# Kernel tuning notes

Hardware: AMD Instinct MI355X
Metric: run time of the kernel (lower is better)

## Reference

```python
import jax, jax.numpy as jnp
import numpy as np

DIM = 512
NUM_HEADS = 8
HEAD_DIM = DIM // NUM_HEADS
SCALE = HEAD_DIM ** -0.5


def setup_inputs() -> dict:
    key = jax.random.key(0)
    k1, k2, k3, k4 = jax.random.split(key, 4)
    x = jax.random.normal(k1, (2, 4096, DIM), dtype=jnp.float32)
    # Linear weights stored as (in, out) for x @ W; torch Linear(dim, 3*dim, bias=False)
    w_qkv = jax.random.normal(k2, (DIM, 3 * DIM), dtype=jnp.float32) * (DIM ** -0.5)
    w_proj = jax.random.normal(k3, (DIM, DIM), dtype=jnp.float32) * (DIM ** -0.5)
    b_proj = jax.random.normal(k4, (DIM,), dtype=jnp.float32) * 0.02
    return {"x": x, "w_qkv": w_qkv, "w_proj": w_proj, "b_proj": b_proj}


def reference(x, w_qkv, w_proj, b_proj):
    B, N, C = x.shape
    qkv = (x @ w_qkv).reshape(B, N, 3, NUM_HEADS, HEAD_DIM)
    qkv = jnp.transpose(qkv, (2, 0, 3, 1, 4))  # (3, B, H, N, hd)
    q, k, v = qkv[0], qkv[1], qkv[2]
    attn = jnp.einsum("bhnd,bhmd->bhnm", q, k) * SCALE
    attn = jax.nn.softmax(attn, axis=-1)
    out = jnp.einsum("bhnm,bhmd->bhnd", attn, v)
    out = jnp.transpose(out, (0, 2, 1, 3)).reshape(B, N, C)
    return out @ w_proj + b_proj
```

## Files before the change

kernel.cpp:

```cpp
#include <hip/hip_runtime.h>
#include <hip/hip_bf16.h>
#include <stdint.h>
#include <math.h>

#define NC3 1536
#define QSCALE 0.18033688011111907f
#define KSPLIT 2

typedef __attribute__((ext_vector_type(8))) short short8;
typedef __attribute__((ext_vector_type(4))) short short4v;
typedef __attribute__((ext_vector_type(4))) float f32x4;
typedef __attribute__((ext_vector_type(16))) float f32x16;
typedef __attribute__((ext_vector_type(8))) _Float16 f16x8;
typedef __attribute__((ext_vector_type(2))) __fp16 fp16x2;

static __device__ __forceinline__ short f2bf(float f) {
    union { __hip_bfloat16 h; short s; } u;
    u.h = __float2bfloat16(f);
    return u.s;
}
static __device__ __forceinline__ float bf2f(short s) {
    return __uint_as_float(((unsigned)(unsigned short)s) << 16);
}
static __device__ __forceinline__ short f2h(float f) {
    union { __fp16 h; short s; } u;
    u.h = (__fp16)f;
    return u.s;
}
static __device__ __forceinline__ unsigned hpack(float a, float b) {
    union { fp16x2 h; unsigned u; } c;
    c.h = __builtin_amdgcn_cvt_pkrtz(a, b);
    return c.u;
}

#define GLD_LDS(g, l)                                                          \
    __builtin_amdgcn_global_load_lds(                                          \
        (const __attribute__((address_space(1))) void*)(g),                    \
        (__attribute__((address_space(3))) void*)(l), 16, 0, 0)

#define GSTRIDE 520
#define LADDR(row, slot) ((((row) >> 3) * GSTRIDE) + (((row) & 7) * 64) + (slot) * 8)

__global__ __launch_bounds__(256) void prep(const float* __restrict__ x,
                                            short* __restrict__ xbf,
                                            const float* __restrict__ wqkv,
                                            short* __restrict__ wqkvT,
                                            const float* __restrict__ wproj,
                                            short* __restrict__ wprojT) {
    int tx = threadIdx.x, ty = threadIdx.y;
    int tid = ty * 32 + tx;
    if (blockIdx.z == 0) {
        int bid = blockIdx.y * 48 + blockIdx.x;
        for (int i = bid * 256 + tid; i < 1048576; i += 768 * 256) {
            float4 v = ((const float4*)x)[i];
            short4v o = {f2bf(v.x), f2bf(v.y), f2bf(v.z), f2bf(v.w)};
            ((short4v*)xbf)[i] = o;
        }
        return;
    }
    const float* src;
    short* dst;
    int C;
    bool tof16;
    if (blockIdx.z == 1) { src = wqkv; dst = wqkvT; C = 1536; tof16 = false; }
    else                 { if (blockIdx.x >= 16) return; src = wproj; dst = wprojT; C = 512; tof16 = true; }
    __shared__ short t[32][33];
    int c0 = blockIdx.x * 32, r0 = blockIdx.y * 32;
#pragma unroll
    for (int i = 0; i < 4; i++) {
        float v = src[(size_t)(r0 + ty + i * 8) * C + c0 + tx];
        t[ty + i * 8][tx] = tof16 ? f2h(v) : f2bf(v);
    }
    __syncthreads();
#pragma unroll
    for (int i = 0; i < 4; i++)
        dst[(size_t)(c0 + ty + i * 8) * 512 + r0 + tx] = t[tx][ty + i * 8];
}

__global__ __launch_bounds__(256) void transpose_v(const short* __restrict__ QKV,
                                                   short* __restrict__ VT) {
    __shared__ short t[32][33];
    int n0 = blockIdx.x * 32, d0 = blockIdx.y * 32;
    int bh = blockIdx.z;
    int b = bh >> 3, h = bh & 7;
    const short* src = QKV + (size_t)b * 4096 * NC3 + 1024 + h * 64;
    short* dst = VT + (size_t)bh * 64 * 4096;
    int tx = threadIdx.x, ty = threadIdx.y;
#pragma unroll
    for (int i = 0; i < 4; i++)
        t[ty + i * 8][tx] = src[(size_t)(n0 + ty + i * 8) * NC3 + d0 + tx];
    __syncthreads();
    int ptx = (tx & ~12) | ((tx & 4) << 1) | ((tx & 8) >> 1);
#pragma unroll
    for (int i = 0; i < 4; i++)
        dst[(size_t)(d0 + ty + i * 8) * 4096 + n0 + ptx] = f2h(bf2f(t[tx][ty + i * 8]));
}

__global__ __launch_bounds__(256) void gemm_qkv(const short* __restrict__ A,
                                                const short* __restrict__ Bt,
                                                short* __restrict__ Out) {
    __shared__ __attribute__((aligned(16))) short a_sm[128 * 64];
    __shared__ __attribute__((aligned(16))) short b_sm[128 * 64];
    const int tid = threadIdx.x;
    const int lane = tid & 63;
    const int wave = tid >> 6;
    const int wr = wave >> 1, wc = wave & 1;
    const int quad = lane >> 4;
    const int l15 = lane & 15;
    const int m0 = blockIdx.x * 128;
    const int n0 = blockIdx.y * 128;
    const int srow = lane >> 3;
    const int schunk = (lane & 7) ^ srow;

    f32x4 zero4 = {0.f, 0.f, 0.f, 0.f};
    f32x4 acc[4][4];
#pragma unroll
    for (int i = 0; i < 4; i++)
#pragma unroll
        for (int j = 0; j < 4; j++) acc[i][j] = zero4;

    for (int k0 = 0; k0 < 512; k0 += 64) {
        __syncthreads();
#pragma unroll
        for (int i = 0; i < 4; i++) {
            int r0 = wave * 32 + i * 8;
            GLD_LDS(A + (size_t)(m0 + r0 + srow) * 512 + k0 + schunk * 8, a_sm + r0 * 64);
            GLD_LDS(Bt + (size_t)(n0 + r0 + srow) * 512 + k0 + schunk * 8, b_sm + r0 * 64);
        }
        __syncthreads();
#pragma unroll
        for (int kk = 0; kk < 2; kk++) {
            short8 af[4], bfr[4];
#pragma unroll
            for (int mi = 0; mi < 4; mi++) {
                int row = wr * 64 + mi * 16 + l15;
                af[mi] = *(const short8*)(a_sm + row * 64 + (((kk * 4 + quad) ^ (row & 7))) * 8);
            }
#pragma unroll
            for (int ni = 0; ni < 4; ni++) {
                int row = wc * 64 + ni * 16 + l15;
                bfr[ni] = *(const short8*)(b_sm + row * 64 + (((kk * 4 + quad) ^ (row & 7))) * 8);
            }
#pragma unroll
            for (int mi = 0; mi < 4; mi++)
#pragma unroll
                for (int ni = 0; ni < 4; ni++)
                    acc[mi][ni] = __builtin_amdgcn_mfma_f32_16x16x32_bf16(
                        af[mi], bfr[ni], acc[mi][ni], 0, 0, 0);
        }
    }

#pragma unroll
    for (int mi = 0; mi < 4; mi++) {
#pragma unroll
        for (int ni = 0; ni < 4; ni++) {
            int gm0 = m0 + wr * 64 + mi * 16 + quad * 4;
            int gn = n0 + wc * 64 + ni * 16 + l15;
            f32x4 v = acc[mi][ni];
#pragma unroll
            for (int r = 0; r < 4; r++) {
                float val = v[r];
                float o = (gn < 512) ? val * QSCALE : val;
                Out[(size_t)(gm0 + r) * NC3 + gn] = f2bf(o);
            }
        }
    }
}

__global__ __launch_bounds__(256, 4) void attn_kernel(const short* __restrict__ QKV,
                                                      const short* __restrict__ VT,
                                                      short* __restrict__ Op0,
                                                      short* __restrict__ Op1,
                                                      float* __restrict__ lpart) {
    __shared__ __attribute__((aligned(16))) short k_sm[2][8 * GSTRIDE];
    __shared__ __attribute__((aligned(16))) short v_sm[2][8 * GSTRIDE];

    const int tid = threadIdx.x;
    const int lane = tid & 63;
    const int wave = tid >> 6;
    const int l31 = lane & 31;
    const int hi = lane >> 5;
    const int qt = blockIdx.x;
    const int bh = blockIdx.y;
    const int ks = blockIdx.z;
    const int b = bh >> 3, h = bh & 7;
    const size_t tokbase = (size_t)b * 4096;
    const int rowbase = qt * 128;
    const int kt0 = ks * (64 / KSPLIT);
    const int kt1 = kt0 + (64 / KSPLIT);
    const short* Qg = QKV + h * 64;
    const short* Kg = QKV + 512 + h * 64;
    const short* VTg = VT + (size_t)bh * 64 * 4096;
    const int srow = lane >> 3;
    const int schunk = (lane & 7) ^ srow;

    short* qstage = &k_sm[0][0];
#pragma unroll
    for (int i = 0; i < 4; i++) {
        int r0 = wave * 32 + i * 8;
        GLD_LDS(Qg + (tokbase + rowbase + r0 + srow) * NC3 + schunk * 8,
                qstage + (r0 >> 3) * GSTRIDE);
    }
    __syncthreads();
    const int qrow = wave * 32 + l31;
    short8 qf[4];
#pragma unroll
    for (int kk = 0; kk < 4; kk++) {
        int slot = (kk * 2 + hi) ^ (qrow & 7);
        qf[kk] = *(const short8*)(qstage + LADDR(qrow, slot));
    }
    __syncthreads();

#pragma unroll
    for (int i = 0; i < 2; i++) {
        int r0 = wave * 16 + i * 8;
        GLD_LDS(Kg + (tokbase + (size_t)kt0 * 64 + r0 + srow) * NC3 + schunk * 8,
                k_sm[0] + (r0 >> 3) * GSTRIDE);
        GLD_LDS(VTg + (size_t)(r0 + srow) * 4096 + kt0 * 64 + schunk * 8,
                v_sm[0] + (r0 >> 3) * GSTRIDE);
    }

    const _Float16 onef = (_Float16)1.0f;
    const f16x8 ones16 = {onef, onef, onef, onef, onef, onef, onef, onef};

    f32x16 acc_o[2], acc_l;
#pragma unroll
    for (int i = 0; i < 16; i++) { acc_o[0][i] = 0.f; acc_o[1][i] = 0.f; acc_l[i] = 0.f; }

    for (int kt = kt0; kt < kt1; kt++) {
        __syncthreads();
        const int cur = kt & 1;
        if (kt < kt1 - 1) {
            const int nb = cur ^ 1;
#pragma unroll
            for (int i = 0; i < 2; i++) {
                int r0 = wave * 16 + i * 8;
                GLD_LDS(Kg + (tokbase + (size_t)(kt + 1) * 64 + r0 + srow) * NC3 + schunk * 8,
                        k_sm[nb] + (r0 >> 3) * GSTRIDE);
                GLD_LDS(VTg + (size_t)(r0 + srow) * 4096 + (kt + 1) * 64 + schunk * 8,
                        v_sm[nb] + (r0 >> 3) * GSTRIDE);
            }
        }

        f32x16 s[2];
#pragma unroll
        for (int i = 0; i < 16; i++) { s[0][i] = 0.f; s[1][i] = 0.f; }
#pragma unroll
        for (int kk = 0; kk < 4; kk++) {
#pragma unroll
            for (int kb = 0; kb < 2; kb++) {
                int row = kb * 32 + l31;
                int slot = (kk * 2 + hi) ^ (row & 7);
                short8 kf = *(const short8*)(k_sm[cur] + LADDR(row, slot));
                s[kb] = __builtin_amdgcn_mfma_f32_32x32x16_bf16(kf, qf[kk], s[kb], 0, 0, 0);
            }
        }

        unsigned pk[2][8];
#pragma unroll
        for (int kb = 0; kb < 2; kb++)
#pragma unroll
            for (int i = 0; i < 16; i += 2)
                pk[kb][i >> 1] = hpack(__builtin_amdgcn_exp2f(s[kb][i]),
                                       __builtin_amdgcn_exp2f(s[kb][i + 1]));

#pragma unroll
        for (int g = 0; g < 4; g++) {
            union { unsigned u[4]; f16x8 v; } pf;
#pragma unroll
            for (int t = 0; t < 4; t++) pf.u[t] = pk[g >> 1][4 * (g & 1) + t];
            acc_l = __builtin_amdgcn_mfma_f32_32x32x16_f16(ones16, pf.v, acc_l, 0, 0, 0);
#pragma unroll
            for (int db = 0; db < 2; db++) {
                int row = db * 32 + l31;
                int slot = (g * 2 + hi) ^ (row & 7);
                f16x8 vf = *(const f16x8*)(v_sm[cur] + LADDR(row, slot));
                acc_o[db] = __builtin_amdgcn_mfma_f32_32x32x16_f16(vf, pf.v, acc_o[db], 0, 0, 0);
            }
        }
    }

    __syncthreads();

    size_t growq = tokbase + rowbase + qrow;
    if (hi == 0) lpart[(size_t)ks * 65536 + growq * 8 + h] = acc_l[0];

    short* osm = &k_sm[0][0] + wave * 2048;
#pragma unroll
    for (int db = 0; db < 2; db++) {
#pragma unroll
        for (int i = 0; i < 16; i += 2) {
            int d = db * 32 + (i & 3) + 8 * (i >> 2) + 4 * hi;
            unsigned pkd = hpack(acc_o[db][i], acc_o[db][i + 1]);
            int slot = (d >> 3) ^ (l31 & 7);
            *(unsigned*)(osm + l31 * 64 + slot * 8 + (d & 7)) = pkd;
        }
    }
    short* Od = (ks == 0) ? Op0 : Op1;
#pragma unroll
    for (int j = 0; j < 4; j++) {
        int r = lane >> 1;
        int c = (lane & 1) * 4 + j;
        int slot = c ^ (r & 7);
        short8 ov = *(const short8*)(osm + r * 64 + slot * 8);
        size_t grow = tokbase + rowbase + wave * 32 + r;
        *(short8*)(Od + grow * 512 + h * 64 + c * 8) = ov;
    }
}

__global__ __launch_bounds__(256) void gemm_proj(const short* __restrict__ Op0,
                                                 const short* __restrict__ Op1,
                                                 const float* __restrict__ lpart,
                                                 const short* __restrict__ Bt,
                                                 float* __restrict__ OutF,
                                                 const float* __restrict__ bias) {
    __shared__ __attribute__((aligned(16))) short a0_sm[128 * 64];
    __shared__ __attribute__((aligned(16))) short a1_sm[128 * 64];
    __shared__ __attribute__((aligned(16))) short b_sm[64 * 64];
    __shared__ float linv_sm[128 * 8];
    const int tid = threadIdx.x;
    const int lane = tid & 63;
    const int wave = tid >> 6;
    const int wr = wave >> 1, wc = wave & 1;
    const int quad = lane >> 4;
    const int l15 = lane & 15;
    const int m0 = blockIdx.x * 128;
    const int n0 = blockIdx.y * 64;
    const int srow = lane >> 3;
    const int schunk = (lane & 7) ^ srow;

    {
        int idx = tid * 4;
        int row = idx >> 3;
        int hh = idx & 7;
        float4 va = *(const float4*)(lpart + (size_t)(m0 + row) * 8 + hh);
        float4 vb = *(const float4*)(lpart + 65536 + (size_t)(m0 + row) * 8 + hh);
        linv_sm[idx + 0] = 1.0f / (va.x + vb.x);
        linv_sm[idx + 1] = 1.0f / (va.y + vb.y);
        linv_sm[idx + 2] = 1.0f / (va.z + vb.z);
        linv_sm[idx + 3] = 1.0f / (va.w + vb.w);
    }

    f32x4 zero4 = {0.f, 0.f, 0.f, 0.f};
    f32x4 acc[4][2];
#pragma unroll
    for (int i = 0; i < 4; i++) { acc[i][0] = zero4; acc[i][1] = zero4; }

    for (int k0 = 0; k0 < 512; k0 += 64) {
        __syncthreads();
#pragma unroll
        for (int i = 0; i < 4; i++) {
            int r0 = wave * 32 + i * 8;
            GLD_LDS(Op0 + (size_t)(m0 + r0 + srow) * 512 + k0 + schunk * 8, a0_sm + r0 * 64);
            GLD_LDS(Op1 + (size_t)(m0 + r0 + srow) * 512 + k0 + schunk * 8, a1_sm + r0 * 64);
        }
#pragma unroll
        for (int i = 0; i < 2; i++) {
            int r0 = wave * 16 + i * 8;
            GLD_LDS(Bt + (size_t)(n0 + r0 + srow) * 512 + k0 + schunk * 8, b_sm + r0 * 64);
        }
        __syncthreads();
        const int h = k0 >> 6;
#pragma unroll
        for (int kk = 0; kk < 2; kk++) {
            f16x8 af[4], bfr[2];
#pragma unroll
            for (int mi = 0; mi < 4; mi++) {
                int row = wr * 64 + mi * 16 + l15;
                int slot = (kk * 4 + quad) ^ (row & 7);
                f16x8 a0v = *(const f16x8*)(a0_sm + row * 64 + slot * 8);
                f16x8 a1v = *(const f16x8*)(a1_sm + row * 64 + slot * 8);
                _Float16 lh = (_Float16)linv_sm[row * 8 + h];
                f16x8 lv = {lh, lh, lh, lh, lh, lh, lh, lh};
                af[mi] = (a0v + a1v) * lv;
            }
#pragma unroll
            for (int ni = 0; ni < 2; ni++) {
                int row = wc * 32 + ni * 16 + l15;
                int slot = (kk * 4 + quad) ^ (row & 7);
                bfr[ni] = *(const f16x8*)(b_sm + row * 64 + slot * 8);
            }
#pragma unroll
            for (int mi = 0; mi < 4; mi++)
#pragma unroll
                for (int ni = 0; ni < 2; ni++)
                    acc[mi][ni] = __builtin_amdgcn_mfma_f32_16x16x32_f16(
                        af[mi], bfr[ni], acc[mi][ni], 0, 0, 0);
        }
    }

#pragma unroll
    for (int mi = 0; mi < 4; mi++) {
#pragma unroll
        for (int ni = 0; ni < 2; ni++) {
            int gm0 = m0 + wr * 64 + mi * 16 + quad * 4;
            int gn = n0 + wc * 32 + ni * 16 + l15;
            f32x4 v = acc[mi][ni];
#pragma unroll
            for (int r = 0; r < 4; r++)
                OutF[(size_t)(gm0 + r) * 512 + gn] = v[r] + bias[gn];
        }
    }
}

extern "C" void kernel_launch(void* const* d_in, const int* in_sizes, int n_in,
                              void* d_out, int out_size, void* d_ws, size_t ws_size,
                              hipStream_t stream) {
    (void)in_sizes; (void)n_in; (void)out_size; (void)ws_size;
    const float* x = (const float*)d_in[0];
    const float* wqkv = (const float*)d_in[1];
    const float* wproj = (const float*)d_in[2];
    const float* bproj = (const float*)d_in[3];
    float* out = (float*)d_out;

    short* ws = (short*)d_ws;
    short* xbf = ws;
    short* wqkvT = xbf + (size_t)4194304;
    short* wprojT = wqkvT + (size_t)1536 * 512;
    short* QKV = wprojT + (size_t)512 * 512;
    short* VTb = QKV + (size_t)8192 * 1536;
    short* Op0 = VTb + (size_t)16 * 64 * 4096;
    short* Op1 = xbf;
    float* lpart = (float*)wqkvT;

    prep<<<dim3(48, 16, 3), dim3(32, 8), 0, stream>>>(x, xbf, wqkv, wqkvT, wproj, wprojT);
    gemm_qkv<<<dim3(64, 12), 256, 0, stream>>>(xbf, wqkvT, QKV);
    transpose_v<<<dim3(128, 2, 16), dim3(32, 8), 0, stream>>>(QKV, VTb);
    attn_kernel<<<dim3(32, 16, KSPLIT), 256, 0, stream>>>(QKV, VTb, Op0, Op1, lpart);
    gemm_proj<<<dim3(64, 8), 256, 0, stream>>>(Op0, Op1, lpart, wprojT, out, bproj);
}
```

Baseline: 201.4 us.

## Fuse V transpose into QKV GEMM epilogue and drop padded LDS stride

```diff
diff --git a/kernel.cpp b/kernel.cpp
--- a/kernel.cpp
+++ b/kernel.cpp
@@ -37,9 +37,6 @@
     __builtin_amdgcn_global_load_lds(                                          \
         (const __attribute__((address_space(1))) void*)(g),                    \
         (__attribute__((address_space(3))) void*)(l), 16, 0, 0)
-
-#define GSTRIDE 520
-#define LADDR(row, slot) ((((row) >> 3) * GSTRIDE) + (((row) & 7) * 64) + (slot) * 8)
 
 __global__ __launch_bounds__(256) void prep(const float* __restrict__ x,
                                             short* __restrict__ xbf,
@@ -77,30 +74,13 @@
         dst[(size_t)(c0 + ty + i * 8) * 512 + r0 + tx] = t[tx][ty + i * 8];
 }
 
-__global__ __launch_bounds__(256) void transpose_v(const short* __restrict__ QKV,
-                                                   short* __restrict__ VT) {
-    __shared__ short t[32][33];
-    int n0 = blockIdx.x * 32, d0 = blockIdx.y * 32;
-    int bh = blockIdx.z;
-    int b = bh >> 3, h = bh & 7;
-    const short* src = QKV + (size_t)b * 4096 * NC3 + 1024 + h * 64;
-    short* dst = VT + (size_t)bh * 64 * 4096;
-    int tx = threadIdx.x, ty = threadIdx.y;
-#pragma unroll
-    for (int i = 0; i < 4; i++)
-        t[ty + i * 8][tx] = src[(size_t)(n0 + ty + i * 8) * NC3 + d0 + tx];
-    __syncthreads();
-    int ptx = (tx & ~12) | ((tx & 4) << 1) | ((tx & 8) >> 1);
-#pragma unroll
-    for (int i = 0; i < 4; i++)
-        dst[(size_t)(d0 + ty + i * 8) * 4096 + n0 + ptx] = f2h(bf2f(t[tx][ty + i * 8]));
-}
-
 __global__ __launch_bounds__(256) void gemm_qkv(const short* __restrict__ A,
                                                 const short* __restrict__ Bt,
-                                                short* __restrict__ Out) {
-    __shared__ __attribute__((aligned(16))) short a_sm[128 * 64];
-    __shared__ __attribute__((aligned(16))) short b_sm[128 * 64];
+                                                short* __restrict__ Out,
+                                                short* __restrict__ VT) {
+    __shared__ __attribute__((aligned(16))) short smem[2][128 * 64];
+    short* a_sm = &smem[0][0];
+    short* b_sm = &smem[1][0];
     const int tid = threadIdx.x;
     const int lane = tid & 63;
     const int wave = tid >> 6;
@@ -165,6 +145,40 @@
             }
         }
     }
+
+    if (n0 >= 1024) {
+        __syncthreads();
+        short* lt = &smem[0][0];
+        const int sq = ((quad & 1) << 1) | (quad >> 1);
+#pragma unroll
+        for (int mi = 0; mi < 4; mi++) {
+#pragma unroll
+            for (int ni = 0; ni < 4; ni++) {
+                int cl = wc * 64 + ni * 16 + l15;
+                int tg = wr * 16 + mi * 4 + sq;
+                int tg2 = tg ^ ((cl & 7) << 1);
+                f32x4 v = acc[mi][ni];
+                uint2 pk;
+                pk.x = hpack(v[0], v[1]);
+                pk.y = hpack(v[2], v[3]);
+                *(uint2*)(lt + cl * 128 + tg2 * 4) = pk;
+            }
+        }
+        __syncthreads();
+        int cl = tid >> 1, half = tid & 1;
+        int cv = n0 - 1024 + cl;
+        int h = cv >> 6, d = cv & 63;
+        int btok = m0 >> 12;
+        int mt = m0 & 4095;
+        short* vrow = VT + ((size_t)((btok * 8 + h) * 64 + d)) * 4096 + mt + half * 64;
+        int m = (cl & 7) << 1;
+#pragma unroll
+        for (int j = 0; j < 8; j++) {
+            int tg = half * 16 + j * 2;
+            short8 v8 = *(const short8*)(lt + cl * 128 + (tg ^ m) * 4);
+            *(short8*)(vrow + j * 8) = v8;
+        }
+    }
 }
 
 __global__ __launch_bounds__(256, 4) void attn_kernel(const short* __restrict__ QKV,
@@ -172,8 +186,8 @@
                                                       short* __restrict__ Op0,
                                                       short* __restrict__ Op1,
                                                       float* __restrict__ lpart) {
-    __shared__ __attribute__((aligned(16))) short k_sm[2][8 * GSTRIDE];
-    __shared__ __attribute__((aligned(16))) short v_sm[2][8 * GSTRIDE];
+    __shared__ __attribute__((aligned(16))) short k_sm[2][64 * 64];
+    __shared__ __attribute__((aligned(16))) short v_sm[2][64 * 64];
 
     const int tid = threadIdx.x;
     const int lane = tid & 63;
@@ -198,8 +212,7 @@
 #pragma unroll
     for (int i = 0; i < 4; i++) {
         int r0 = wave * 32 + i * 8;
-        GLD_LDS(Qg + (tokbase + rowbase + r0 + srow) * NC3 + schunk * 8,
-                qstage + (r0 >> 3) * GSTRIDE);
+        GLD_LDS(Qg + (tokbase + rowbase + r0 + srow) * NC3 + schunk * 8, qstage + r0 * 64);
     }
     __syncthreads();
     const int qrow = wave * 32 + l31;
@@ -207,7 +220,7 @@
 #pragma unroll
     for (int kk = 0; kk < 4; kk++) {
         int slot = (kk * 2 + hi) ^ (qrow & 7);
-        qf[kk] = *(const short8*)(qstage + LADDR(qrow, slot));
+        qf[kk] = *(const short8*)(qstage + qrow * 64 + slot * 8);
     }
     __syncthreads();
 
@@ -215,9 +228,9 @@
     for (int i = 0; i < 2; i++) {
         int r0 = wave * 16 + i * 8;
         GLD_LDS(Kg + (tokbase + (size_t)kt0 * 64 + r0 + srow) * NC3 + schunk * 8,
-                k_sm[0] + (r0 >> 3) * GSTRIDE);
+                k_sm[0] + r0 * 64);
         GLD_LDS(VTg + (size_t)(r0 + srow) * 4096 + kt0 * 64 + schunk * 8,
-                v_sm[0] + (r0 >> 3) * GSTRIDE);
+                v_sm[0] + r0 * 64);
     }
 
     const _Float16 onef = (_Float16)1.0f;
@@ -236,9 +249,9 @@
             for (int i = 0; i < 2; i++) {
                 int r0 = wave * 16 + i * 8;
                 GLD_LDS(Kg + (tokbase + (size_t)(kt + 1) * 64 + r0 + srow) * NC3 + schunk * 8,
-                        k_sm[nb] + (r0 >> 3) * GSTRIDE);
+                        k_sm[nb] + r0 * 64);
                 GLD_LDS(VTg + (size_t)(r0 + srow) * 4096 + (kt + 1) * 64 + schunk * 8,
-                        v_sm[nb] + (r0 >> 3) * GSTRIDE);
+                        v_sm[nb] + r0 * 64);
             }
         }
 
@@ -251,7 +264,7 @@
             for (int kb = 0; kb < 2; kb++) {
                 int row = kb * 32 + l31;
                 int slot = (kk * 2 + hi) ^ (row & 7);
-                short8 kf = *(const short8*)(k_sm[cur] + LADDR(row, slot));
+                short8 kf = *(const short8*)(k_sm[cur] + row * 64 + slot * 8);
                 s[kb] = __builtin_amdgcn_mfma_f32_32x32x16_bf16(kf, qf[kk], s[kb], 0, 0, 0);
             }
         }
@@ -274,7 +287,7 @@
             for (int db = 0; db < 2; db++) {
                 int row = db * 32 + l31;
                 int slot = (g * 2 + hi) ^ (row & 7);
-                f16x8 vf = *(const f16x8*)(v_sm[cur] + LADDR(row, slot));
+                f16x8 vf = *(const f16x8*)(v_sm[cur] + row * 64 + slot * 8);
                 acc_o[db] = __builtin_amdgcn_mfma_f32_32x32x16_f16(vf, pf.v, acc_o[db], 0, 0, 0);
             }
         }
@@ -424,8 +437,7 @@
     float* lpart = (float*)wqkvT;
 
     prep<<<dim3(48, 16, 3), dim3(32, 8), 0, stream>>>(x, xbf, wqkv, wqkvT, wproj, wprojT);
-    gemm_qkv<<<dim3(64, 12), 256, 0, stream>>>(xbf, wqkvT, QKV);
-    transpose_v<<<dim3(128, 2, 16), dim3(32, 8), 0, stream>>>(QKV, VTb);
+    gemm_qkv<<<dim3(64, 12), 256, 0, stream>>>(xbf, wqkvT, QKV, VTb);
     attn_kernel<<<dim3(32, 16, KSPLIT), 256, 0, stream>>>(QKV, VTb, Op0, Op1, lpart);
     gemm_proj<<<dim3(64, 8), 256, 0, stream>>>(Op0, Op1, lpart, wprojT, out, bproj);
 }
```

New measurement: 197.8 us. About the same (-1.8%).
